# Kernel optimization log

Hardware: AMD Instinct MI355X
Metric: run time of the kernel (lower is better)

## Reference

```python
import jax, jax.numpy as jnp
import numpy as np

N = 80000      # points (voxels)
M = 2048       # windows
C = 128        # d_model
H = 8          # heads
D = C // H     # head_dim = 16
B = 2          # batch size
HB, WB = 32, 32  # BEV window grid shape


def setup_inputs() -> dict:
    key = jax.random.key(0)
    k1, k2, k3, k4 = jax.random.split(key, 4)
    x = jax.random.normal(k1, (N, C), dtype=jnp.float32)
    Wqkv = jax.random.normal(k2, (3 * C, C), dtype=jnp.float32) * 0.05
    Wproj = jax.random.normal(k3, (C, C), dtype=jnp.float32) * 0.05
    bproj = jax.random.normal(k4, (C,), dtype=jnp.float32) * 0.05
    # ragged windows: near-equal contiguous split of N into M groups
    base = N // M
    rem = N - base * M
    counts_np = base + (np.arange(M) < rem).astype(np.int64)
    offsets_np = np.concatenate([[0], np.cumsum(counts_np)[:-1]]).astype(np.int64)
    batch_win_inds_np = np.repeat(np.arange(M, dtype=np.int64), counts_np)
    wid = np.arange(M, dtype=np.int64)
    coords_np = np.stack([wid // (HB * WB), (wid % (HB * WB)) // WB, wid % WB], axis=1)
    return {
        "x": x, "Wqkv": Wqkv, "Wproj": Wproj, "bproj": bproj,
        "offsets": jnp.asarray(offsets_np), "counts": jnp.asarray(counts_np),
        "batch_win_inds": jnp.asarray(batch_win_inds_np),
        "batch_win_coords": jnp.asarray(coords_np),
    }


def _pool3x3(feat, coords):
    # sparse 3x3 sum-pool (stride 1, pad 1) over BEV grid, via dense scatter + shifted sums
    F_ = feat.shape[-1]
    grid = jnp.zeros((B, HB, WB, F_), feat.dtype).at[coords[:, 0], coords[:, 1], coords[:, 2]].set(feat)
    p = jnp.pad(grid, ((0, 0), (1, 1), (1, 1), (0, 0)))
    pooled = sum(p[:, dy:dy + HB, dx:dx + WB] for dy in range(3) for dx in range(3))
    return pooled[coords[:, 0], coords[:, 1], coords[:, 2]]


def reference(x, Wqkv, Wproj, bproj, offsets, counts, batch_win_inds, batch_win_coords):
    n = x.shape[0]
    qkv = (x @ Wqkv.T).reshape(n, 3, H, D)
    q = jax.nn.relu(qkv[:, 0])  # [N, H, D]
    k = jax.nn.relu(qkv[:, 1])
    v = qkv[:, 2]
    # per-window cumulative K^T V (scatter_matmul_kv): [M, H, D, D]
    kv_pt = jnp.einsum('nhd,nhe->nhde', k, v)
    kv = jax.ops.segment_sum(kv_pt, batch_win_inds, num_segments=M)
    # per-window key sum: [M, H, D]
    s = jax.ops.segment_sum(k, batch_win_inds, num_segments=M)
    # 3x3 sum pool over neighboring windows
    kv = _pool3x3(kv.reshape(M, H * D * D), batch_win_coords).reshape(M, H, D, D)
    s = _pool3x3(s.reshape(M, H * D), batch_win_coords).reshape(M, H, D)
    # Q @ C readout (scatter_matmul_qc)
    y = jnp.einsum('nhd,nhde->nhe', q, kv[batch_win_inds])
    z = jnp.sum(s[batch_win_inds] * q, axis=-1, keepdims=True)
    y = y / (z + 1e-6)
    y = y.reshape(n, C)
    return y @ Wproj.T + bproj
```

## Files before the change

kernel.cpp:

```cpp
#include <hip/hip_runtime.h>

#define MWIN 2048
#define HH 8

typedef _Float16 half8 __attribute__((ext_vector_type(8)));
typedef _Float16 half4 __attribute__((ext_vector_type(4)));
typedef float f32x4 __attribute__((ext_vector_type(4)));

__global__ __launch_bounds__(256) void k_prep(const float* __restrict__ x,
                                              _Float16* __restrict__ x_f, int nxt,
                                              int N,
                                              const float* __restrict__ Wqkv,
                                              const float* __restrict__ Wproj,
                                              _Float16* __restrict__ fq,
                                              _Float16* __restrict__ fp) {
    int bid = blockIdx.x;
    if (bid < 32) {
        int tid = bid * 256 + threadIdx.x;
        const float* src;
        _Float16* dst;
        if (tid < 6144) { src = Wqkv; dst = fq; }
        else {
            tid -= 6144;
            if (tid >= 2048) return;
            src = Wproj; dst = fp;
        }
        int lane = tid & 63, r = tid >> 6;
        int ct = r & 3, ks = (r >> 2) & 3, cg = r >> 4;
        int m = lane & 15, q = lane >> 4;
        const float* s_ = src + (size_t)(cg * 64 + ct * 16 + m) * 128 + q * 8 + ks * 32;
        float4 f0 = *(const float4*)s_;
        float4 f1 = *(const float4*)(s_ + 4);
        half8 h;
        h[0] = (_Float16)f0.x; h[1] = (_Float16)f0.y; h[2] = (_Float16)f0.z; h[3] = (_Float16)f0.w;
        h[4] = (_Float16)f1.x; h[5] = (_Float16)f1.y; h[6] = (_Float16)f1.z; h[7] = (_Float16)f1.w;
        *(half8*)(dst + (size_t)tid * 8) = h;
        return;
    }
    int i = (bid - 32) * 256 + threadIdx.x;
    if (i >= nxt) return;
    int lane = i & 63, ks = (i >> 6) & 3, t = i >> 8;
    int m = lane & 15, q = lane >> 4;
    int row = t * 16 + m;
    row = row < N ? row : N - 1;
    const float* s_ = x + (size_t)row * 128 + q * 8 + ks * 32;
    float4 f0 = *(const float4*)s_;
    float4 f1 = *(const float4*)(s_ + 4);
    half8 h;
    h[0] = (_Float16)f0.x; h[1] = (_Float16)f0.y; h[2] = (_Float16)f0.z; h[3] = (_Float16)f0.w;
    h[4] = (_Float16)f1.x; h[5] = (_Float16)f1.y; h[6] = (_Float16)f1.z; h[7] = (_Float16)f1.w;
    *(half8*)(x_f + (size_t)i * 8) = h;
}

template <int CGS, bool RELU>
__global__ __launch_bounds__(256) void k_mfma_gemm(const half8* __restrict__ Afrag,
                                                   const half8* __restrict__ Bfrag,
                                                   _Float16* __restrict__ out, int ldo,
                                                   int N) {
    __shared__ float st[4][32][68];
    int tid = threadIdx.x;
    int lane = tid & 63, wv = tid >> 6;
    int m = lane & 15, q = lane >> 4;
    int row0 = blockIdx.x * 256 + wv * 64;
    float (*stw)[68] = st[wv];

    half8 a[4][4];
    #pragma unroll
    for (int rt = 0; rt < 4; ++rt) {
        int t = (row0 >> 4) + rt;
        #pragma unroll
        for (int ks = 0; ks < 4; ++ks)
            a[rt][ks] = Afrag[((size_t)t * 4 + ks) * 64 + lane];
    }

    #pragma unroll
    for (int cgi = 0; cgi < CGS; ++cgi) {
        int cgG = blockIdx.y * CGS + cgi;
        int col0 = cgG * 64;
        f32x4 acc[4][4];
        #pragma unroll
        for (int ct = 0; ct < 4; ++ct)
            #pragma unroll
            for (int rt = 0; rt < 4; ++rt) acc[rt][ct] = (f32x4){0.f, 0.f, 0.f, 0.f};
        #pragma unroll
        for (int ks = 0; ks < 4; ++ks) {
            half8 b[4];
            #pragma unroll
            for (int ct = 0; ct < 4; ++ct)
                b[ct] = Bfrag[((size_t)cgG * 16 + ks * 4 + ct) * 64 + lane];
            #pragma unroll
            for (int rt = 0; rt < 4; ++rt)
                #pragma unroll
                for (int ct = 0; ct < 4; ++ct)
                    acc[rt][ct] = __builtin_amdgcn_mfma_f32_16x16x32_f16(a[rt][ks], b[ct], acc[rt][ct], 0, 0, 0);
        }
        #pragma unroll
        for (int hp = 0; hp < 2; ++hp) {
            #pragma unroll
            for (int rh = 0; rh < 2; ++rh) {
                int rt = hp * 2 + rh;
                #pragma unroll
                for (int reg = 0; reg < 4; ++reg) {
                    int lr = rh * 16 + q * 4 + reg;
                    #pragma unroll
                    for (int ct = 0; ct < 4; ++ct)
                        stw[lr][ct * 16 + m] = acc[rt][ct][reg];
                }
            }
            #pragma unroll
            for (int ps = 0; ps < 4; ++ps) {
                int r = ps * 8 + (lane >> 3), c0 = (lane & 7) * 8;
                float4 f0 = *(const float4*)&stw[r][c0];
                float4 f1 = *(const float4*)&stw[r][c0 + 4];
                if (RELU && (col0 + c0) < 256) {
                    f0.x = fmaxf(f0.x, 0.f); f0.y = fmaxf(f0.y, 0.f);
                    f0.z = fmaxf(f0.z, 0.f); f0.w = fmaxf(f0.w, 0.f);
                    f1.x = fmaxf(f1.x, 0.f); f1.y = fmaxf(f1.y, 0.f);
                    f1.z = fmaxf(f1.z, 0.f); f1.w = fmaxf(f1.w, 0.f);
                }
                half8 h;
                h[0] = (_Float16)f0.x; h[1] = (_Float16)f0.y;
                h[2] = (_Float16)f0.z; h[3] = (_Float16)f0.w;
                h[4] = (_Float16)f1.x; h[5] = (_Float16)f1.y;
                h[6] = (_Float16)f1.z; h[7] = (_Float16)f1.w;
                int grow = row0 + hp * 32 + r;
                if (grow < N)
                    *(half8*)(out + (size_t)grow * ldo + col0 + c0) = h;
            }
        }
    }
}

__global__ __launch_bounds__(512) void k_kv_accum(const _Float16* __restrict__ qkv,
                                                  const int* __restrict__ offsets,
                                                  const int* __restrict__ counts,
                                                  float* __restrict__ kv_t,
                                                  float* __restrict__ s) {
    __shared__ _Float16 kvl[40][256];
    int w = blockIdx.x;
    int off = offsets[w], cnt = counts[w];
    int tid = threadIdx.x;
    for (int base = 0; base < cnt; base += 16) {
        int p = base + (tid >> 5);
        if (p < cnt)
            *(half8*)&kvl[p][(tid & 31) * 8] =
                *(const half8*)(qkv + (size_t)(off + p) * 384 + 128 + (tid & 31) * 8);
    }
    __syncthreads();
    int h = tid >> 6, lane = tid & 63;
    int d = lane & 15, eq = lane >> 4;
    float a0 = 0.f, a1 = 0.f, a2 = 0.f, a3 = 0.f, sa = 0.f;
    for (int p = 0; p < cnt; ++p) {
        float kk = (float)kvl[p][h * 16 + d];
        half4 v4 = *(const half4*)&kvl[p][128 + h * 16 + eq * 4];
        a0 += kk * (float)v4[0];
        a1 += kk * (float)v4[1];
        a2 += kk * (float)v4[2];
        a3 += kk * (float)v4[3];
        sa += kk;
    }
    float* o = kv_t + (((size_t)(w * HH + h)) << 8);
    o[(eq * 4 + 0) * 16 + d] = a0;
    o[(eq * 4 + 1) * 16 + d] = a1;
    o[(eq * 4 + 2) * 16 + d] = a2;
    o[(eq * 4 + 3) * 16 + d] = a3;
    if (eq == 0) s[(((size_t)(w * HH + h)) << 4) + d] = sa;
}

__global__ __launch_bounds__(512) void k_attn_proj(const _Float16* __restrict__ qkv,
                                                   const float* __restrict__ kv_t,
                                                   const float* __restrict__ s,
                                                   const half8* __restrict__ fp,
                                                   const float* __restrict__ bproj,
                                                   const int* __restrict__ offsets,
                                                   const int* __restrict__ counts,
                                                   float* __restrict__ out) {
    __shared__ _Float16 y_t[48][136];
    __shared__ float o_t[48][132];
    int w = blockIdx.x;
    int h = threadIdx.x >> 6;
    int lane = threadIdx.x & 63;
    int col = lane & 15;
    int kq = lane >> 4;
    int off = offsets[w], cnt = counts[w];
    bool klive = kq < 2;
    int koff = (kq & 1) * 8;

    int b = w >> 10, yy = (w >> 5) & 31, xx = w & 31;
    f32x4 k0 = {}, k1 = {}, s0 = {}, s1 = {};
    if (klive) {
        #pragma unroll
        for (int dy = -1; dy <= 1; ++dy)
            #pragma unroll
            for (int dx = -1; dx <= 1; ++dx) {
                int ny = yy + dy, nx = xx + dx;
                if (ny < 0 || ny >= 32 || nx < 0 || nx >= 32) continue;
                int nw = (b << 10) | (ny << 5) | nx;
                const float* kb = kv_t + (((size_t)(nw * HH + h)) << 8) + col * 16 + koff;
                k0 += *(const f32x4*)kb;
                k1 += *(const f32x4*)(kb + 4);
                const float* sb = s + (((size_t)(nw * HH + h)) << 4) + koff;
                s0 += *(const f32x4*)sb;
                s1 += *(const f32x4*)(sb + 4);
            }
    }
    half8 a_kv, a_s;
    #pragma unroll
    for (int i = 0; i < 4; ++i) {
        a_kv[i] = (_Float16)k0[i]; a_kv[4 + i] = (_Float16)k1[i];
        a_s[i]  = (_Float16)s0[i]; a_s[4 + i]  = (_Float16)s1[i];
    }

    #pragma unroll
    for (int c = 0; c < 3; ++c) {
        int p = c * 16 + col;
        int pc = p < cnt ? p : cnt - 1;
        half8 b_q = *(const half8*)(qkv + (size_t)(off + pc) * 384 + h * 16 + koff);
        f32x4 acc = {};
        acc = __builtin_amdgcn_mfma_f32_16x16x32_f16(a_kv, b_q, acc, 0, 0, 0);
        f32x4 accs = {};
        accs = __builtin_amdgcn_mfma_f32_16x16x32_f16(a_s, b_q, accs, 0, 0, 0);
        float zinv = 1.f / (accs[0] + 1e-6f);
        half4 yo;
        #pragma unroll
        for (int i = 0; i < 4; ++i) yo[i] = (_Float16)(acc[i] * zinv);
        *(half4*)&y_t[p][h * 16 + kq * 4] = yo;
    }
    __syncthreads();

    int m = col, q = kq;
    int ct = h;
    int cg = ct >> 2, ctl = ct & 3;
    half8 bfr[4];
    #pragma unroll
    for (int ks = 0; ks < 4; ++ks)
        bfr[ks] = fp[((size_t)cg * 16 + ks * 4 + ctl) * 64 + lane];
    float bv = bproj[ct * 16 + m];
    #pragma unroll
    for (int rt = 0; rt < 3; ++rt) {
        f32x4 acc = (f32x4){bv, bv, bv, bv};
        #pragma unroll
        for (int ks = 0; ks < 4; ++ks) {
            half8 af = *(const half8*)&y_t[rt * 16 + m][q * 8 + ks * 32];
            acc = __builtin_amdgcn_mfma_f32_16x16x32_f16(af, bfr[ks], acc, 0, 0, 0);
        }
        #pragma unroll
        for (int reg = 0; reg < 4; ++reg)
            o_t[rt * 16 + q * 4 + reg][ct * 16 + m] = acc[reg];
    }
    __syncthreads();

    #pragma unroll
    for (int it = 0; it < 3; ++it) {
        int j = it * 512 + threadIdx.x;
        int r = j >> 5, c4 = j & 31;
        if (r < cnt)
            *(float4*)(out + ((size_t)(off + r) << 7) + c4 * 4) = *(const float4*)&o_t[r][c4 * 4];
    }
}

extern "C" void kernel_launch(void* const* d_in, const int* in_sizes, int n_in,
                              void* d_out, int out_size, void* d_ws, size_t ws_size,
                              hipStream_t stream) {
    const float* x     = (const float*)d_in[0];
    const float* Wqkv  = (const float*)d_in[1];
    const float* Wproj = (const float*)d_in[2];
    const float* bproj = (const float*)d_in[3];
    const int*   offsets = (const int*)d_in[4];
    const int*   counts  = (const int*)d_in[5];

    int N = in_sizes[0] / 128;
    int nrb = (N + 255) / 256;
    int Npad = nrb * 256;

    char* ws = (char*)d_ws;
    float* kv_t = (float*)ws;                                    ws += (size_t)MWIN * HH * 256 * 4;
    float* s    = (float*)ws;                                    ws += (size_t)MWIN * HH * 16 * 4;
    _Float16* x_f    = (_Float16*)ws;                            ws += (size_t)Npad * 128 * 2;
    _Float16* qkv_h  = (_Float16*)ws;                            ws += (size_t)N * 384 * 2;
    _Float16* fq     = (_Float16*)ws;                            ws += (size_t)6144 * 8 * 2;
    _Float16* fp     = (_Float16*)ws;                            ws += (size_t)2048 * 8 * 2;
    float* out  = (float*)d_out;

    int nxt = Npad * 16;
    k_prep<<<32 + (nxt + 255) / 256, 256, 0, stream>>>(x, x_f, nxt, N, Wqkv, Wproj, fq, fp);

    k_mfma_gemm<2, true><<<dim3(nrb, 3), 256, 0, stream>>>(
        (const half8*)x_f, (const half8*)fq, qkv_h, 384, N);

    k_kv_accum<<<MWIN, 512, 0, stream>>>(qkv_h, offsets, counts, kv_t, s);

    k_attn_proj<<<MWIN, 512, 0, stream>>>(qkv_h, kv_t, s, (const half8*)fp, bproj,
                                          offsets, counts, out);
}
```

Measured before the change: 178.5 us.

## Fuse QKV projection into per-window KV accumulation kernel, store only Q

```diff
diff --git a/kernel.cpp b/kernel.cpp
--- a/kernel.cpp
+++ b/kernel.cpp
@@ -7,152 +7,106 @@
 typedef _Float16 half4 __attribute__((ext_vector_type(4)));
 typedef float f32x4 __attribute__((ext_vector_type(4)));
 
-__global__ __launch_bounds__(256) void k_prep(const float* __restrict__ x,
-                                              _Float16* __restrict__ x_f, int nxt,
-                                              int N,
-                                              const float* __restrict__ Wqkv,
-                                              const float* __restrict__ Wproj,
-                                              _Float16* __restrict__ fq,
-                                              _Float16* __restrict__ fp) {
-    int bid = blockIdx.x;
-    if (bid < 32) {
-        int tid = bid * 256 + threadIdx.x;
-        const float* src;
-        _Float16* dst;
-        if (tid < 6144) { src = Wqkv; dst = fq; }
-        else {
-            tid -= 6144;
-            if (tid >= 2048) return;
-            src = Wproj; dst = fp;
-        }
-        int lane = tid & 63, r = tid >> 6;
-        int ct = r & 3, ks = (r >> 2) & 3, cg = r >> 4;
-        int m = lane & 15, q = lane >> 4;
-        const float* s_ = src + (size_t)(cg * 64 + ct * 16 + m) * 128 + q * 8 + ks * 32;
-        float4 f0 = *(const float4*)s_;
-        float4 f1 = *(const float4*)(s_ + 4);
-        half8 h;
-        h[0] = (_Float16)f0.x; h[1] = (_Float16)f0.y; h[2] = (_Float16)f0.z; h[3] = (_Float16)f0.w;
-        h[4] = (_Float16)f1.x; h[5] = (_Float16)f1.y; h[6] = (_Float16)f1.z; h[7] = (_Float16)f1.w;
-        *(half8*)(dst + (size_t)tid * 8) = h;
-        return;
-    }
-    int i = (bid - 32) * 256 + threadIdx.x;
-    if (i >= nxt) return;
-    int lane = i & 63, ks = (i >> 6) & 3, t = i >> 8;
+__device__ __forceinline__ int win_swz(int bid) {
+    return (bid & 7) * 256 + (bid >> 3);
+}
+
+__global__ __launch_bounds__(256) void k_prep_w(const float* __restrict__ Wqkv,
+                                                const float* __restrict__ Wproj,
+                                                _Float16* __restrict__ fq,
+                                                _Float16* __restrict__ fp) {
+    int tid = blockIdx.x * 256 + threadIdx.x;
+    const float* src;
+    _Float16* dst;
+    if (tid < 6144) { src = Wqkv; dst = fq; }
+    else {
+        tid -= 6144;
+        if (tid >= 2048) return;
+        src = Wproj; dst = fp;
+    }
+    int lane = tid & 63, r = tid >> 6;
+    int ct = r & 3, ks = (r >> 2) & 3, cg = r >> 4;
     int m = lane & 15, q = lane >> 4;
-    int row = t * 16 + m;
-    row = row < N ? row : N - 1;
-    const float* s_ = x + (size_t)row * 128 + q * 8 + ks * 32;
+    const float* s_ = src + (size_t)(cg * 64 + ct * 16 + m) * 128 + q * 8 + ks * 32;
     float4 f0 = *(const float4*)s_;
     float4 f1 = *(const float4*)(s_ + 4);
     half8 h;
     h[0] = (_Float16)f0.x; h[1] = (_Float16)f0.y; h[2] = (_Float16)f0.z; h[3] = (_Float16)f0.w;
     h[4] = (_Float16)f1.x; h[5] = (_Float16)f1.y; h[6] = (_Float16)f1.z; h[7] = (_Float16)f1.w;
-    *(half8*)(x_f + (size_t)i * 8) = h;
-}
-
-template <int CGS, bool RELU>
-__global__ __launch_bounds__(256) void k_mfma_gemm(const half8* __restrict__ Afrag,
-                                                   const half8* __restrict__ Bfrag,
-                                                   _Float16* __restrict__ out, int ldo,
-                                                   int N) {
-    __shared__ float st[4][32][68];
+    *(half8*)(dst + (size_t)tid * 8) = h;
+}
+
+__global__ __launch_bounds__(512) void k_qkv_win(const float* __restrict__ x,
+                                                 const half8* __restrict__ fq,
+                                                 const int* __restrict__ offsets,
+                                                 const int* __restrict__ counts,
+                                                 _Float16* __restrict__ q_h,
+                                                 float* __restrict__ kv_t,
+                                                 float* __restrict__ s) {
+    __shared__ _Float16 qk[48][392];
+    int w = win_swz(blockIdx.x);
+    int off = offsets[w], cnt = counts[w];
     int tid = threadIdx.x;
-    int lane = tid & 63, wv = tid >> 6;
+    int h = tid >> 6, lane = tid & 63;
     int m = lane & 15, q = lane >> 4;
-    int row0 = blockIdx.x * 256 + wv * 64;
-    float (*stw)[68] = st[wv];
-
-    half8 a[4][4];
-    #pragma unroll
-    for (int rt = 0; rt < 4; ++rt) {
-        int t = (row0 >> 4) + rt;
+
+    half8 a[3][4];
+    #pragma unroll
+    for (int rt = 0; rt < 3; ++rt) {
+        int r = rt * 16 + m;
+        r = r < cnt ? r : cnt - 1;
+        const float* ap = x + (size_t)(off + r) * 128 + q * 8;
+        #pragma unroll
+        for (int ks = 0; ks < 4; ++ks) {
+            float4 f0 = *(const float4*)(ap + ks * 32);
+            float4 f1 = *(const float4*)(ap + ks * 32 + 4);
+            half8 hh;
+            hh[0] = (_Float16)f0.x; hh[1] = (_Float16)f0.y;
+            hh[2] = (_Float16)f0.z; hh[3] = (_Float16)f0.w;
+            hh[4] = (_Float16)f1.x; hh[5] = (_Float16)f1.y;
+            hh[6] = (_Float16)f1.z; hh[7] = (_Float16)f1.w;
+            a[rt][ks] = hh;
+        }
+    }
+
+    #pragma unroll
+    for (int j = 0; j < 3; ++j) {
+        int ctg = h * 3 + j;
+        int cg = ctg >> 2, ctl = ctg & 3;
+        half8 bfr[4];
         #pragma unroll
         for (int ks = 0; ks < 4; ++ks)
-            a[rt][ks] = Afrag[((size_t)t * 4 + ks) * 64 + lane];
-    }
-
-    #pragma unroll
-    for (int cgi = 0; cgi < CGS; ++cgi) {
-        int cgG = blockIdx.y * CGS + cgi;
-        int col0 = cgG * 64;
-        f32x4 acc[4][4];
-        #pragma unroll
-        for (int ct = 0; ct < 4; ++ct)
+            bfr[ks] = fq[((size_t)cg * 16 + ks * 4 + ctl) * 64 + lane];
+        bool dorelu = ctg < 16;
+        #pragma unroll
+        for (int rt = 0; rt < 3; ++rt) {
+            f32x4 acc = {};
             #pragma unroll
-            for (int rt = 0; rt < 4; ++rt) acc[rt][ct] = (f32x4){0.f, 0.f, 0.f, 0.f};
-        #pragma unroll
-        for (int ks = 0; ks < 4; ++ks) {
-            half8 b[4];
+            for (int ks = 0; ks < 4; ++ks)
+                acc = __builtin_amdgcn_mfma_f32_16x16x32_f16(a[rt][ks], bfr[ks], acc, 0, 0, 0);
             #pragma unroll
-            for (int ct = 0; ct < 4; ++ct)
-                b[ct] = Bfrag[((size_t)cgG * 16 + ks * 4 + ct) * 64 + lane];
-            #pragma unroll
-            for (int rt = 0; rt < 4; ++rt)
-                #pragma unroll
-                for (int ct = 0; ct < 4; ++ct)
-                    acc[rt][ct] = __builtin_amdgcn_mfma_f32_16x16x32_f16(a[rt][ks], b[ct], acc[rt][ct], 0, 0, 0);
-        }
-        #pragma unroll
-        for (int hp = 0; hp < 2; ++hp) {
-            #pragma unroll
-            for (int rh = 0; rh < 2; ++rh) {
-                int rt = hp * 2 + rh;
-                #pragma unroll
-                for (int reg = 0; reg < 4; ++reg) {
-                    int lr = rh * 16 + q * 4 + reg;
-                    #pragma unroll
-                    for (int ct = 0; ct < 4; ++ct)
-                        stw[lr][ct * 16 + m] = acc[rt][ct][reg];
-                }
-            }
-            #pragma unroll
-            for (int ps = 0; ps < 4; ++ps) {
-                int r = ps * 8 + (lane >> 3), c0 = (lane & 7) * 8;
-                float4 f0 = *(const float4*)&stw[r][c0];
-                float4 f1 = *(const float4*)&stw[r][c0 + 4];
-                if (RELU && (col0 + c0) < 256) {
-                    f0.x = fmaxf(f0.x, 0.f); f0.y = fmaxf(f0.y, 0.f);
-                    f0.z = fmaxf(f0.z, 0.f); f0.w = fmaxf(f0.w, 0.f);
-                    f1.x = fmaxf(f1.x, 0.f); f1.y = fmaxf(f1.y, 0.f);
-                    f1.z = fmaxf(f1.z, 0.f); f1.w = fmaxf(f1.w, 0.f);
-                }
-                half8 h;
-                h[0] = (_Float16)f0.x; h[1] = (_Float16)f0.y;
-                h[2] = (_Float16)f0.z; h[3] = (_Float16)f0.w;
-                h[4] = (_Float16)f1.x; h[5] = (_Float16)f1.y;
-                h[6] = (_Float16)f1.z; h[7] = (_Float16)f1.w;
-                int grow = row0 + hp * 32 + r;
-                if (grow < N)
-                    *(half8*)(out + (size_t)grow * ldo + col0 + c0) = h;
+            for (int reg = 0; reg < 4; ++reg) {
+                float vv = acc[reg];
+                if (dorelu) vv = fmaxf(vv, 0.f);
+                qk[rt * 16 + q * 4 + reg][ctg * 16 + m] = (_Float16)vv;
             }
         }
     }
-}
-
-__global__ __launch_bounds__(512) void k_kv_accum(const _Float16* __restrict__ qkv,
-                                                  const int* __restrict__ offsets,
-                                                  const int* __restrict__ counts,
-                                                  float* __restrict__ kv_t,
-                                                  float* __restrict__ s) {
-    __shared__ _Float16 kvl[40][256];
-    int w = blockIdx.x;
-    int off = offsets[w], cnt = counts[w];
-    int tid = threadIdx.x;
-    for (int base = 0; base < cnt; base += 16) {
-        int p = base + (tid >> 5);
-        if (p < cnt)
-            *(half8*)&kvl[p][(tid & 31) * 8] =
-                *(const half8*)(qkv + (size_t)(off + p) * 384 + 128 + (tid & 31) * 8);
-    }
     __syncthreads();
-    int h = tid >> 6, lane = tid & 63;
+
+    #pragma unroll
+    for (int it = 0; it < 2; ++it) {
+        int idx = it * 512 + tid;
+        int row = idx >> 4, c8 = idx & 15;
+        if (row < cnt)
+            *(half8*)(q_h + (size_t)(off + row) * 128 + c8 * 8) = *(const half8*)&qk[row][c8 * 8];
+    }
+
     int d = lane & 15, eq = lane >> 4;
     float a0 = 0.f, a1 = 0.f, a2 = 0.f, a3 = 0.f, sa = 0.f;
     for (int p = 0; p < cnt; ++p) {
-        float kk = (float)kvl[p][h * 16 + d];
-        half4 v4 = *(const half4*)&kvl[p][128 + h * 16 + eq * 4];
+        float kk = (float)qk[p][128 + h * 16 + d];
+        half4 v4 = *(const half4*)&qk[p][256 + h * 16 + eq * 4];
         a0 += kk * (float)v4[0];
         a1 += kk * (float)v4[1];
         a2 += kk * (float)v4[2];
@@ -167,7 +121,7 @@
     if (eq == 0) s[(((size_t)(w * HH + h)) << 4) + d] = sa;
 }
 
-__global__ __launch_bounds__(512) void k_attn_proj(const _Float16* __restrict__ qkv,
+__global__ __launch_bounds__(512) void k_attn_proj(const _Float16* __restrict__ q_h,
                                                    const float* __restrict__ kv_t,
                                                    const float* __restrict__ s,
                                                    const half8* __restrict__ fp,
@@ -177,7 +131,7 @@
                                                    float* __restrict__ out) {
     __shared__ _Float16 y_t[48][136];
     __shared__ float o_t[48][132];
-    int w = blockIdx.x;
+    int w = win_swz(blockIdx.x);
     int h = threadIdx.x >> 6;
     int lane = threadIdx.x & 63;
     int col = lane & 15;
@@ -215,7 +169,7 @@
     for (int c = 0; c < 3; ++c) {
         int p = c * 16 + col;
         int pc = p < cnt ? p : cnt - 1;
-        half8 b_q = *(const half8*)(qkv + (size_t)(off + pc) * 384 + h * 16 + koff);
+        half8 b_q = *(const half8*)(q_h + (size_t)(off + pc) * 128 + h * 16 + koff);
         f32x4 acc = {};
         acc = __builtin_amdgcn_mfma_f32_16x16x32_f16(a_kv, b_q, acc, 0, 0, 0);
         f32x4 accs = {};
@@ -270,26 +224,20 @@
     const int*   counts  = (const int*)d_in[5];
 
     int N = in_sizes[0] / 128;
-    int nrb = (N + 255) / 256;
-    int Npad = nrb * 256;
 
     char* ws = (char*)d_ws;
     float* kv_t = (float*)ws;                                    ws += (size_t)MWIN * HH * 256 * 4;
     float* s    = (float*)ws;                                    ws += (size_t)MWIN * HH * 16 * 4;
-    _Float16* x_f    = (_Float16*)ws;                            ws += (size_t)Npad * 128 * 2;
-    _Float16* qkv_h  = (_Float16*)ws;                            ws += (size_t)N * 384 * 2;
+    _Float16* q_h    = (_Float16*)ws;                            ws += (size_t)N * 128 * 2;
     _Float16* fq     = (_Float16*)ws;                            ws += (size_t)6144 * 8 * 2;
     _Float16* fp     = (_Float16*)ws;                            ws += (size_t)2048 * 8 * 2;
     float* out  = (float*)d_out;
 
-    int nxt = Npad * 16;
-    k_prep<<<32 + (nxt + 255) / 256, 256, 0, stream>>>(x, x_f, nxt, N, Wqkv, Wproj, fq, fp);
-
-    k_mfma_gemm<2, true><<<dim3(nrb, 3), 256, 0, stream>>>(
-        (const half8*)x_f, (const half8*)fq, qkv_h, 384, N);
-
-    k_kv_accum<<<MWIN, 512, 0, stream>>>(qkv_h, offsets, counts, kv_t, s);
-
-    k_attn_proj<<<MWIN, 512, 0, stream>>>(qkv_h, kv_t, s, (const half8*)fp, bproj,
+    k_prep_w<<<32, 256, 0, stream>>>(Wqkv, Wproj, fq, fp);
+
+    k_qkv_win<<<MWIN, 512, 0, stream>>>(x, (const half8*)fq, offsets, counts,
+                                        q_h, kv_t, s);
+
+    k_attn_proj<<<MWIN, 512, 0, stream>>>(q_h, kv_t, s, (const half8*)fp, bproj,
                                           offsets, counts, out);
 }
```

After: 179.0 us. About the same (+0.3%).
